# Kernel tuning notes

Measured on AMD Instinct MI355X. Metric: run time of the kernel, lower is better.

## Reference

```python
import jax, jax.numpy as jnp
import numpy as np

K = 5  # neighbors per node


def build_knn_adjacency(x, k=K):
    # x: (B, N, D) -> adj: (B, N, N)
    B, N, D = x.shape
    x_norm = x / jnp.clip(jnp.linalg.norm(x, axis=-1, keepdims=True), 1e-12)
    sim = jnp.einsum('bnd,bmd->bnm', x_norm, x_norm)  # (B, N, N)
    eye = jnp.eye(N, dtype=bool)
    sim = jnp.where(eye[None], jnp.asarray(-1.0, sim.dtype), sim)
    _, knn_idx = jax.lax.top_k(sim, k)  # (B, N, k)
    b_ix = jnp.arange(B)[:, None, None]
    i_ix = jnp.arange(N)[None, :, None]
    adj = jnp.zeros((B, N, N), dtype=x.dtype).at[b_ix, i_ix, knn_idx].set(1.0)
    adj = adj + jnp.eye(N, dtype=x.dtype)[None]
    return adj


def gcn_layer(x, adj, W, b):
    # deg-normalized aggregation then linear (torch Linear: x @ W.T + b)
    deg = adj.sum(axis=-1, keepdims=True)
    adj_norm = adj / jnp.clip(deg, 1.0)
    out = jnp.einsum('bnm,bmd->bnd', adj_norm, x)
    return out @ W.T + b


def setup_inputs() -> dict:
    key = jax.random.key(0)
    k1, k2, k3, k4, k5 = jax.random.split(key, 5)
    B, N, D, H = 32, 1024, 128, 128
    scale = 1.0 / np.sqrt(D)
    return {
        'x': jax.random.normal(k1, (B, N, D), dtype=jnp.float32),
        'W1': jax.random.normal(k2, (H, D), dtype=jnp.float32) * scale,
        'b1': jax.random.normal(k3, (H,), dtype=jnp.float32) * 0.01,
        'W2': jax.random.normal(k4, (H, H), dtype=jnp.float32) * scale,
        'b2': jax.random.normal(k5, (H,), dtype=jnp.float32) * 0.01,
    }


def reference(x, W1, b1, W2, b2):
    adj = build_knn_adjacency(x, k=K)
    h = x + jax.nn.relu(gcn_layer(x, adj, W1, b1))
    h = h + jax.nn.relu(gcn_layer(h, adj, W2, b2))
    return h  # pool='none' -> (B, N, hidden_dim)
```

## Files before the change

### kernel.cpp

```cpp
#include <hip/hip_runtime.h>
#include <float.h>
#include <math.h>

#define BB 32
#define NN 1024
#define DD 128
#define KK 5

typedef __attribute__((ext_vector_type(8))) short bf16x8;
typedef __attribute__((ext_vector_type(4))) float f32x4;

__device__ __forceinline__ unsigned short f2bf(float f) {
    unsigned int u = __float_as_uint(f);
    return (unsigned short)((u + 0x7FFFu + ((u >> 16) & 1u)) >> 16);
}
__device__ __forceinline__ float bf2f(unsigned short h) {
    return __uint_as_float(((unsigned int)h) << 16);
}

__global__ __launch_bounds__(256) void k_norm(const float* __restrict__ x,
                                              unsigned short* __restrict__ ph,
                                              unsigned short* __restrict__ pm,
                                              unsigned short* __restrict__ pl) {
    int row  = blockIdx.x * 4 + (threadIdx.x >> 6);
    int lane = threadIdx.x & 63;
    float2 v = *reinterpret_cast<const float2*>(x + (size_t)row * DD + lane * 2);
    float ss = v.x * v.x + v.y * v.y;
#pragma unroll
    for (int o = 32; o >= 1; o >>= 1) ss += __shfl_xor(ss, o);
    float inv = 1.0f / fmaxf(sqrtf(ss), 1e-12f);
    float y0 = v.x * inv, y1 = v.y * inv;

    unsigned short h0 = f2bf(y0);             float r0 = y0 - bf2f(h0);
    unsigned short m0 = f2bf(r0);             float s0 = r0 - bf2f(m0);
    unsigned short l0 = f2bf(s0);
    unsigned short h1 = f2bf(y1);             float r1 = y1 - bf2f(h1);
    unsigned short m1 = f2bf(r1);             float s1 = r1 - bf2f(m1);
    unsigned short l1 = f2bf(s1);

    size_t o = (size_t)row * DD + lane * 2;
    *reinterpret_cast<unsigned int*>(ph + o) = (unsigned int)h0 | ((unsigned int)h1 << 16);
    *reinterpret_cast<unsigned int*>(pm + o) = (unsigned int)m0 | ((unsigned int)m1 << 16);
    *reinterpret_cast<unsigned int*>(pl + o) = (unsigned int)l0 | ((unsigned int)l1 << 16);
}

union SMem {
    struct {
        unsigned short Ah[128][40], Am[128][40], Al[128][40];
        unsigned short Bh[128][40], Bm[128][40], Bl[128][40];
    } s;
    float q[4][32][68];
};

__device__ __forceinline__ void stage_plane(const unsigned short* __restrict__ g,
                                            unsigned short (*s)[40], int tid,
                                            size_t rowbase, int c) {
#pragma unroll
    for (int hh = 0; hh < 2; ++hh) {
        int u = tid + (hh << 8);
        int row = u >> 2, qq = u & 3;
        const float4 v = *reinterpret_cast<const float4*>(
            g + (rowbase + row) * DD + (c << 5) + (qq << 3));
        *reinterpret_cast<float4*>(&s[row][qq << 3]) = v;
    }
}

__global__ __launch_bounds__(256, 2) void k_sim(const unsigned short* __restrict__ ph,
                                                const unsigned short* __restrict__ pm,
                                                const unsigned short* __restrict__ pl,
                                                float* __restrict__ sim) {
    int bid = blockIdx.x;
    int lb  = (bid & 7) * 144 + (bid >> 3);
    int bl  = lb / 36;
    int p   = lb - bl * 36;
    int ti = 0;
    while (p >= 8 - ti) { p -= 8 - ti; ++ti; }
    int tj = ti + p;
    int R  = ti << 7, Cc = tj << 7;

    __shared__ SMem sm;

    int tid  = threadIdx.x;
    int wv   = tid >> 6;
    int lane = tid & 63;
    int wr = (wv >> 1) << 6;
    int wc = (wv & 1) << 6;
    int lg = lane >> 4, fr = lane & 15;

    size_t base = (size_t)bl * NN;
    size_t rbA = base + R, rbB = base + Cc;

    f32x4 acc[4][4];
#pragma unroll
    for (int i = 0; i < 4; ++i)
#pragma unroll
        for (int j = 0; j < 4; ++j) acc[i][j] = (f32x4){0.f, 0.f, 0.f, 0.f};

    int kk = lg << 3;

    for (int c = 0; c < 4; ++c) {
        if (c) __syncthreads();
        stage_plane(ph, sm.s.Ah, tid, rbA, c);
        stage_plane(pm, sm.s.Am, tid, rbA, c);
        stage_plane(pl, sm.s.Al, tid, rbA, c);
        stage_plane(ph, sm.s.Bh, tid, rbB, c);
        stage_plane(pm, sm.s.Bm, tid, rbB, c);
        stage_plane(pl, sm.s.Bl, tid, rbB, c);
        __syncthreads();

        bf16x8 bh[4], bm[4], blo[4];
#pragma unroll
        for (int cp = 0; cp < 4; ++cp) {
            int rb = wc + cp * 16 + fr;
            bh[cp]  = *reinterpret_cast<const bf16x8*>(&sm.s.Bh[rb][kk]);
            bm[cp]  = *reinterpret_cast<const bf16x8*>(&sm.s.Bm[rb][kk]);
            blo[cp] = *reinterpret_cast<const bf16x8*>(&sm.s.Bl[rb][kk]);
        }
#pragma unroll
        for (int rp = 0; rp < 4; ++rp) {
            int ra = wr + rp * 16 + fr;
            bf16x8 ah = *reinterpret_cast<const bf16x8*>(&sm.s.Ah[ra][kk]);
            bf16x8 am = *reinterpret_cast<const bf16x8*>(&sm.s.Am[ra][kk]);
            bf16x8 al = *reinterpret_cast<const bf16x8*>(&sm.s.Al[ra][kk]);
#pragma unroll
            for (int cp = 0; cp < 4; ++cp) {
                f32x4 cacc = acc[rp][cp];
                cacc = __builtin_amdgcn_mfma_f32_16x16x32_bf16(ah, bh[cp],  cacc, 0, 0, 0);
                cacc = __builtin_amdgcn_mfma_f32_16x16x32_bf16(ah, bm[cp],  cacc, 0, 0, 0);
                cacc = __builtin_amdgcn_mfma_f32_16x16x32_bf16(am, bh[cp],  cacc, 0, 0, 0);
                cacc = __builtin_amdgcn_mfma_f32_16x16x32_bf16(ah, blo[cp], cacc, 0, 0, 0);
                cacc = __builtin_amdgcn_mfma_f32_16x16x32_bf16(al, bh[cp],  cacc, 0, 0, 0);
                cacc = __builtin_amdgcn_mfma_f32_16x16x32_bf16(am, bm[cp],  cacc, 0, 0, 0);
                acc[rp][cp] = cacc;
            }
        }
    }

    __syncthreads();
    float (*q)[68] = sm.q[wv];
    float* Cb = sim + base * NN;

    if (ti != tj) {
#pragma unroll
        for (int hp = 0; hp < 2; ++hp) {
#pragma unroll
            for (int rp = 0; rp < 4; ++rp)
#pragma unroll
                for (int cpl = 0; cpl < 2; ++cpl) {
                    const f32x4 a = acc[rp][2 * hp + cpl];
                    *reinterpret_cast<float4*>(&q[cpl * 16 + fr][rp * 16 + lg * 4]) =
                        make_float4(a[0], a[1], a[2], a[3]);
                }
#pragma unroll
            for (int it = 0; it < 8; ++it) {
                int lcol = lg + 4 * it;
                const float4 v = *reinterpret_cast<const float4*>(&q[lcol][fr * 4]);
                *reinterpret_cast<float4*>(
                    &Cb[(size_t)(Cc + wc + 32 * hp + lcol) * NN + R + wr + fr * 4]) = v;
            }
        }
    }
#pragma unroll
    for (int hr = 0; hr < 2; ++hr) {
#pragma unroll
        for (int rpl = 0; rpl < 2; ++rpl)
#pragma unroll
            for (int cp = 0; cp < 4; ++cp)
#pragma unroll
                for (int reg = 0; reg < 4; ++reg)
                    q[rpl * 16 + lg * 4 + reg][cp * 16 + fr] = acc[2 * hr + rpl][cp][reg];
#pragma unroll
        for (int it = 0; it < 8; ++it) {
            int lrow = lg + 4 * it;
            const float4 v = *reinterpret_cast<const float4*>(&q[lrow][fr * 4]);
            *reinterpret_cast<float4*>(
                &Cb[(size_t)(R + wr + 32 * hr + lrow) * NN + Cc + wc + fr * 4]) = v;
        }
    }
}

__global__ __launch_bounds__(256) void k_topk(const float* __restrict__ sim,
                                              int* __restrict__ idx) {
    int lrow = blockIdx.x * 4 + (threadIdx.x >> 6);
    int lane = threadIdx.x & 63;
    const float* sr = sim + (size_t)lrow * NN;
    int i = lrow & (NN - 1);

    float v[16];
#pragma unroll
    for (int q = 0; q < 4; ++q) {
        float4 f = *reinterpret_cast<const float4*>(sr + lane * 16 + q * 4);
        v[q * 4 + 0] = f.x; v[q * 4 + 1] = f.y; v[q * 4 + 2] = f.z; v[q * 4 + 3] = f.w;
    }
    if ((i >> 4) == lane) {
        int s = i & 15;
#pragma unroll
        for (int j = 0; j < 16; ++j) if (j == s) v[j] = -FLT_MAX;
    }
    int* op = idx + (size_t)lrow * KK;
#pragma unroll
    for (int t = 0; t < KK; ++t) {
        float bv = v[0]; int bj = 0;
#pragma unroll
        for (int j = 1; j < 16; ++j) if (v[j] > bv) { bv = v[j]; bj = j; }
        int bm = (lane << 4) + bj;
#pragma unroll
        for (int o = 1; o < 64; o <<= 1) {
            float ov = __shfl_xor(bv, o);
            int   om = __shfl_xor(bm, o);
            if (ov > bv || (ov == bv && om < bm)) { bv = ov; bm = om; }
        }
        if ((bm >> 4) == lane) {
            int s = bm & 15;
#pragma unroll
            for (int j = 0; j < 16; ++j) if (j == s) v[j] = -FLT_MAX;
        }
        if (lane == 0) op[t] = bm;
    }
}

#define SW(c) ((c) + 4 * ((c) >> 5))

__global__ __launch_bounds__(256, 3) void k_gcn(const float* __restrict__ h,
                                                const int* __restrict__ idx,
                                                const float* __restrict__ W,
                                                const float* __restrict__ bias,
                                                const float* __restrict__ res,
                                                float* __restrict__ out) {
    int rt = blockIdx.x << 6;
    __shared__ float As[64][132];
    __shared__ float Bs[32][140];
    int tid = threadIdx.x;

    {
        int row = tid >> 2, fq = tid & 3;
        int grow = rt + row;
        const int* ip = idx + (size_t)grow * KK;
        const float* hb = h + (((size_t)grow >> 10) << 10) * DD;
        const float* hs = h + (size_t)grow * DD;
        int n0 = ip[0], n1 = ip[1], n2 = ip[2], n3 = ip[3], n4 = ip[4];
        const float* p0 = hb + (size_t)n0 * DD;
        const float* p1 = hb + (size_t)n1 * DD;
        const float* p2 = hb + (size_t)n2 * DD;
        const float* p3 = hb + (size_t)n3 * DD;
        const float* p4 = hb + (size_t)n4 * DD;
        const float cc = 1.0f / 6.0f;
#pragma unroll
        for (int rep = 0; rep < 8; ++rep) {
            int c = rep * 16 + fq * 4;
            float4 v  = *reinterpret_cast<const float4*>(hs + c);
            float4 u0 = *reinterpret_cast<const float4*>(p0 + c);
            float4 u1 = *reinterpret_cast<const float4*>(p1 + c);
            float4 u2 = *reinterpret_cast<const float4*>(p2 + c);
            float4 u3 = *reinterpret_cast<const float4*>(p3 + c);
            float4 u4 = *reinterpret_cast<const float4*>(p4 + c);
            v.x = (v.x + u0.x + u1.x + u2.x + u3.x + u4.x) * cc;
            v.y = (v.y + u0.y + u1.y + u2.y + u3.y + u4.y) * cc;
            v.z = (v.z + u0.z + u1.z + u2.z + u3.z + u4.z) * cc;
            v.w = (v.w + u0.w + u1.w + u2.w + u3.w + u4.w) * cc;
            *reinterpret_cast<float4*>(&As[row][c]) = v;
        }
    }

    int tr  = (tid >> 4) << 2;
    int tc  = (tid & 15) << 3;
    int stc = SW(tc);

    float acc[4][8];
#pragma unroll
    for (int i = 0; i < 4; ++i)
#pragma unroll
        for (int j = 0; j < 8; ++j) acc[i][j] = 0.f;

    for (int kc = 0; kc < 4; ++kc) {
        __syncthreads();
        {
            int hcol = tid >> 1, kq = tid & 1;
            int swc = SW(hcol);
#pragma unroll
            for (int rep = 0; rep < 4; ++rep) {
                int f4i = rep * 2 + kq;
                const float4 v = *reinterpret_cast<const float4*>(
                    W + (size_t)hcol * DD + kc * 32 + f4i * 4);
                int k = f4i * 4;
                Bs[k + 0][swc] = v.x; Bs[k + 1][swc] = v.y;
                Bs[k + 2][swc] = v.z; Bs[k + 3][swc] = v.w;
            }
        }
        __syncthreads();
#pragma unroll 4
        for (int k = 0; k < 32; ++k) {
            int ck = kc * 32 + k;
            const float av[4] = {As[tr + 0][ck], As[tr + 1][ck],
                                 As[tr + 2][ck], As[tr + 3][ck]};
            const float4 b0 = *reinterpret_cast<const float4*>(&Bs[k][stc]);
            const float4 b1 = *reinterpret_cast<const float4*>(&Bs[k][stc + 4]);
            const float bw[8] = {b0.x, b0.y, b0.z, b0.w, b1.x, b1.y, b1.z, b1.w};
#pragma unroll
            for (int ii = 0; ii < 4; ++ii)
#pragma unroll
                for (int jj = 0; jj < 8; ++jj)
                    acc[ii][jj] = fmaf(av[ii], bw[jj], acc[ii][jj]);
        }
    }
    const float4 bz0 = *reinterpret_cast<const float4*>(bias + tc);
    const float4 bz1 = *reinterpret_cast<const float4*>(bias + tc + 4);
    const float bb[8] = {bz0.x, bz0.y, bz0.z, bz0.w, bz1.x, bz1.y, bz1.z, bz1.w};
#pragma unroll
    for (int i = 0; i < 4; ++i) {
        size_t ro = (size_t)(rt + tr + i) * DD + tc;
        const float4 r0 = *reinterpret_cast<const float4*>(res + ro);
        const float4 r1 = *reinterpret_cast<const float4*>(res + ro + 4);
        float4 o0, o1;
        o0.x = r0.x + fmaxf(acc[i][0] + bb[0], 0.f);
        o0.y = r0.y + fmaxf(acc[i][1] + bb[1], 0.f);
        o0.z = r0.z + fmaxf(acc[i][2] + bb[2], 0.f);
        o0.w = r0.w + fmaxf(acc[i][3] + bb[3], 0.f);
        o1.x = r1.x + fmaxf(acc[i][4] + bb[4], 0.f);
        o1.y = r1.y + fmaxf(acc[i][5] + bb[5], 0.f);
        o1.z = r1.z + fmaxf(acc[i][6] + bb[6], 0.f);
        o1.w = r1.w + fmaxf(acc[i][7] + bb[7], 0.f);
        *reinterpret_cast<float4*>(out + ro)     = o0;
        *reinterpret_cast<float4*>(out + ro + 4) = o1;
    }
}

extern "C" void kernel_launch(void* const* d_in, const int* in_sizes, int n_in,
                              void* d_out, int out_size, void* d_ws, size_t ws_size,
                              hipStream_t stream) {
    const float* x  = (const float*)d_in[0];
    const float* W1 = (const float*)d_in[1];
    const float* b1 = (const float*)d_in[2];
    const float* W2 = (const float*)d_in[3];
    const float* b2 = (const float*)d_in[4];
    float* out = (float*)d_out;

    char* ws = (char*)d_ws;
    size_t pl_b  = (size_t)BB * NN * DD * 2;
    size_t h1_b  = (size_t)BB * NN * DD * 4;
    size_t idx_b = (size_t)BB * NN * KK * 4;
    unsigned short* ph = (unsigned short*)ws;  ws += pl_b;
    unsigned short* pm = (unsigned short*)ws;  ws += pl_b;
    unsigned short* pl = (unsigned short*)ws;  ws += pl_b;
    float* h1  = (float*)ws;                   ws += h1_b;
    int*   idx = (int*)ws;                     ws += idx_b;
    float* sim = (float*)ws;

    k_norm<<<BB * NN / 4, 256, 0, stream>>>(x, ph, pm, pl);
    k_sim<<<BB * 36, 256, 0, stream>>>(ph, pm, pl, sim);
    k_topk<<<BB * NN / 4, 256, 0, stream>>>(sim, idx);
    k_gcn<<<BB * NN / 64, 256, 0, stream>>>(x,  idx, W1, b1, x,  h1);
    k_gcn<<<BB * NN / 64, 256, 0, stream>>>(h1, idx, W2, b2, h1, out);
}
```

Measured before the change: 156.6 us.

## Fuse partial top-k into similarity kernel and merge candidates instead of storing sim

The similarity GEMM kernel no longer writes the full B×N×N similarity matrix. Each wave computes a per-row top-5 over its 64-column slice, for both the tile and its transpose, and writes packed 64-bit keys (value, column) as candidates. A new small merge kernel then reduces the 16 candidate lists per row to the final top-5 indices. This removes the 128MB sim write and reread, at the cost of extra shuffle and selection work in the GEMM epilogue.

```diff
diff --git a/kernel.cpp b/kernel.cpp
--- a/kernel.cpp
+++ b/kernel.cpp
@@ -9,6 +9,7 @@
 
 typedef __attribute__((ext_vector_type(8))) short bf16x8;
 typedef __attribute__((ext_vector_type(4))) float f32x4;
+typedef unsigned long long ull;
 
 __device__ __forceinline__ unsigned short f2bf(float f) {
     unsigned int u = __float_as_uint(f);
@@ -16,6 +17,12 @@
 }
 __device__ __forceinline__ float bf2f(unsigned short h) {
     return __uint_as_float(((unsigned int)h) << 16);
+}
+
+__device__ __forceinline__ ull mkkey(float v, int col) {
+    unsigned int u = __float_as_uint(v);
+    unsigned int ou = u ^ (unsigned)((((int)u) >> 31) | 0x80000000);
+    return ((ull)ou << 32) | (unsigned)(1023 - col);
 }
 
 __global__ __launch_bounds__(256) void k_norm(const float* __restrict__ x,
@@ -44,14 +51,6 @@
     *reinterpret_cast<unsigned int*>(pl + o) = (unsigned int)l0 | ((unsigned int)l1 << 16);
 }
 
-union SMem {
-    struct {
-        unsigned short Ah[128][40], Am[128][40], Al[128][40];
-        unsigned short Bh[128][40], Bm[128][40], Bl[128][40];
-    } s;
-    float q[4][32][68];
-};
-
 __device__ __forceinline__ void stage_plane(const unsigned short* __restrict__ g,
                                             unsigned short (*s)[40], int tid,
                                             size_t rowbase, int c) {
@@ -68,7 +67,7 @@
 __global__ __launch_bounds__(256, 2) void k_sim(const unsigned short* __restrict__ ph,
                                                 const unsigned short* __restrict__ pm,
                                                 const unsigned short* __restrict__ pl,
-                                                float* __restrict__ sim) {
+                                                ull* __restrict__ cand) {
     int bid = blockIdx.x;
     int lb  = (bid & 7) * 144 + (bid >> 3);
     int bl  = lb / 36;
@@ -78,7 +77,10 @@
     int tj = ti + p;
     int R  = ti << 7, Cc = tj << 7;
 
-    __shared__ SMem sm;
+    __shared__ struct {
+        unsigned short Ah[128][40], Am[128][40], Al[128][40];
+        unsigned short Bh[128][40], Bm[128][40], Bl[128][40];
+    } sm;
 
     int tid  = threadIdx.x;
     int wv   = tid >> 6;
@@ -100,28 +102,28 @@
 
     for (int c = 0; c < 4; ++c) {
         if (c) __syncthreads();
-        stage_plane(ph, sm.s.Ah, tid, rbA, c);
-        stage_plane(pm, sm.s.Am, tid, rbA, c);
-        stage_plane(pl, sm.s.Al, tid, rbA, c);
-        stage_plane(ph, sm.s.Bh, tid, rbB, c);
-        stage_plane(pm, sm.s.Bm, tid, rbB, c);
-        stage_plane(pl, sm.s.Bl, tid, rbB, c);
+        stage_plane(ph, sm.Ah, tid, rbA, c);
+        stage_plane(pm, sm.Am, tid, rbA, c);
+        stage_plane(pl, sm.Al, tid, rbA, c);
+        stage_plane(ph, sm.Bh, tid, rbB, c);
+        stage_plane(pm, sm.Bm, tid, rbB, c);
+        stage_plane(pl, sm.Bl, tid, rbB, c);
         __syncthreads();
 
         bf16x8 bh[4], bm[4], blo[4];
 #pragma unroll
         for (int cp = 0; cp < 4; ++cp) {
             int rb = wc + cp * 16 + fr;
-            bh[cp]  = *reinterpret_cast<const bf16x8*>(&sm.s.Bh[rb][kk]);
-            bm[cp]  = *reinterpret_cast<const bf16x8*>(&sm.s.Bm[rb][kk]);
-            blo[cp] = *reinterpret_cast<const bf16x8*>(&sm.s.Bl[rb][kk]);
+            bh[cp]  = *reinterpret_cast<const bf16x8*>(&sm.Bh[rb][kk]);
+            bm[cp]  = *reinterpret_cast<const bf16x8*>(&sm.Bm[rb][kk]);
+            blo[cp] = *reinterpret_cast<const bf16x8*>(&sm.Bl[rb][kk]);
         }
 #pragma unroll
         for (int rp = 0; rp < 4; ++rp) {
             int ra = wr + rp * 16 + fr;
-            bf16x8 ah = *reinterpret_cast<const bf16x8*>(&sm.s.Ah[ra][kk]);
-            bf16x8 am = *reinterpret_cast<const bf16x8*>(&sm.s.Am[ra][kk]);
-            bf16x8 al = *reinterpret_cast<const bf16x8*>(&sm.s.Al[ra][kk]);
+            bf16x8 ah = *reinterpret_cast<const bf16x8*>(&sm.Ah[ra][kk]);
+            bf16x8 am = *reinterpret_cast<const bf16x8*>(&sm.Am[ra][kk]);
+            bf16x8 al = *reinterpret_cast<const bf16x8*>(&sm.Al[ra][kk]);
 #pragma unroll
             for (int cp = 0; cp < 4; ++cp) {
                 f32x4 cacc = acc[rp][cp];
@@ -136,86 +138,107 @@
         }
     }
 
-    __syncthreads();
-    float (*q)[68] = sm.q[wv];
-    float* Cb = sim + base * NN;
+    {
+        int slotR = 2 * tj + (wc >> 6);
+        int c0 = Cc + wc + fr;
+#pragma unroll
+        for (int rp = 0; rp < 4; ++rp) {
+#pragma unroll
+            for (int reg = 0; reg < 4; ++reg) {
+                int grow = R + wr + rp * 16 + lg * 4 + reg;
+                float v0 = acc[rp][0][reg], v1 = acc[rp][1][reg];
+                float v2 = acc[rp][2][reg], v3 = acc[rp][3][reg];
+                if (ti == tj) {
+                    v0 = (c0      == grow) ? -FLT_MAX : v0;
+                    v1 = (c0 + 16 == grow) ? -FLT_MAX : v1;
+                    v2 = (c0 + 32 == grow) ? -FLT_MAX : v2;
+                    v3 = (c0 + 48 == grow) ? -FLT_MAX : v3;
+                }
+                ull w[5];
+#pragma unroll
+                for (int t = 0; t < 5; ++t) {
+                    float bv = v0; int bc = c0;
+                    if (v1 > bv) { bv = v1; bc = c0 + 16; }
+                    if (v2 > bv) { bv = v2; bc = c0 + 32; }
+                    if (v3 > bv) { bv = v3; bc = c0 + 48; }
+#pragma unroll
+                    for (int o = 1; o < 16; o <<= 1) {
+                        float ov = __shfl_xor(bv, o);
+                        int   oc = __shfl_xor(bc, o);
+                        if (ov > bv || (ov == bv && oc < bc)) { bv = ov; bc = oc; }
+                    }
+                    w[t] = mkkey(bv, bc);
+                    v0 = (bc == c0)      ? -FLT_MAX : v0;
+                    v1 = (bc == c0 + 16) ? -FLT_MAX : v1;
+                    v2 = (bc == c0 + 32) ? -FLT_MAX : v2;
+                    v3 = (bc == c0 + 48) ? -FLT_MAX : v3;
+                }
+                if (fr == 0) {
+                    ull* o = cand + ((base + grow) * 16 + slotR) * 5;
+                    o[0] = w[0]; o[1] = w[1]; o[2] = w[2]; o[3] = w[3]; o[4] = w[4];
+                }
+            }
+        }
+    }
 
     if (ti != tj) {
-#pragma unroll
-        for (int hp = 0; hp < 2; ++hp) {
+        int slotM = 2 * ti + (wr >> 6);
+        int nbase = R + wr + lg * 4;
+#pragma unroll
+        for (int cp = 0; cp < 4; ++cp) {
+            float mv[16];
 #pragma unroll
             for (int rp = 0; rp < 4; ++rp)
 #pragma unroll
-                for (int cpl = 0; cpl < 2; ++cpl) {
-                    const f32x4 a = acc[rp][2 * hp + cpl];
-                    *reinterpret_cast<float4*>(&q[cpl * 16 + fr][rp * 16 + lg * 4]) =
-                        make_float4(a[0], a[1], a[2], a[3]);
-                }
-#pragma unroll
-            for (int it = 0; it < 8; ++it) {
-                int lcol = lg + 4 * it;
-                const float4 v = *reinterpret_cast<const float4*>(&q[lcol][fr * 4]);
-                *reinterpret_cast<float4*>(
-                    &Cb[(size_t)(Cc + wc + 32 * hp + lcol) * NN + R + wr + fr * 4]) = v;
-            }
-        }
-    }
-#pragma unroll
-    for (int hr = 0; hr < 2; ++hr) {
-#pragma unroll
-        for (int rpl = 0; rpl < 2; ++rpl)
-#pragma unroll
-            for (int cp = 0; cp < 4; ++cp)
-#pragma unroll
                 for (int reg = 0; reg < 4; ++reg)
-                    q[rpl * 16 + lg * 4 + reg][cp * 16 + fr] = acc[2 * hr + rpl][cp][reg];
-#pragma unroll
-        for (int it = 0; it < 8; ++it) {
-            int lrow = lg + 4 * it;
-            const float4 v = *reinterpret_cast<const float4*>(&q[lrow][fr * 4]);
-            *reinterpret_cast<float4*>(
-                &Cb[(size_t)(R + wr + 32 * hr + lrow) * NN + Cc + wc + fr * 4]) = v;
-        }
-    }
-}
-
-__global__ __launch_bounds__(256) void k_topk(const float* __restrict__ sim,
-                                              int* __restrict__ idx) {
-    int lrow = blockIdx.x * 4 + (threadIdx.x >> 6);
-    int lane = threadIdx.x & 63;
-    const float* sr = sim + (size_t)lrow * NN;
-    int i = lrow & (NN - 1);
-
-    float v[16];
-#pragma unroll
-    for (int q = 0; q < 4; ++q) {
-        float4 f = *reinterpret_cast<const float4*>(sr + lane * 16 + q * 4);
-        v[q * 4 + 0] = f.x; v[q * 4 + 1] = f.y; v[q * 4 + 2] = f.z; v[q * 4 + 3] = f.w;
-    }
-    if ((i >> 4) == lane) {
-        int s = i & 15;
-#pragma unroll
-        for (int j = 0; j < 16; ++j) if (j == s) v[j] = -FLT_MAX;
-    }
-    int* op = idx + (size_t)lrow * KK;
-#pragma unroll
-    for (int t = 0; t < KK; ++t) {
-        float bv = v[0]; int bj = 0;
-#pragma unroll
-        for (int j = 1; j < 16; ++j) if (v[j] > bv) { bv = v[j]; bj = j; }
-        int bm = (lane << 4) + bj;
-#pragma unroll
-        for (int o = 1; o < 64; o <<= 1) {
-            float ov = __shfl_xor(bv, o);
-            int   om = __shfl_xor(bm, o);
-            if (ov > bv || (ov == bv && om < bm)) { bv = ov; bm = om; }
-        }
-        if ((bm >> 4) == lane) {
-            int s = bm & 15;
-#pragma unroll
-            for (int j = 0; j < 16; ++j) if (j == s) v[j] = -FLT_MAX;
-        }
-        if (lane == 0) op[t] = bm;
+                    mv[rp * 4 + reg] = acc[rp][cp][reg];
+            ull w[5];
+#pragma unroll
+            for (int t = 0; t < 5; ++t) {
+                float bv = mv[0]; int bn = nbase;
+#pragma unroll
+                for (int e = 1; e < 16; ++e) {
+                    int n = nbase + (e >> 2) * 16 + (e & 3);
+                    if (mv[e] > bv) { bv = mv[e]; bn = n; }
+                }
+                {   float ov = __shfl_xor(bv, 16); int on = __shfl_xor(bn, 16);
+                    if (ov > bv || (ov == bv && on < bn)) { bv = ov; bn = on; } }
+                {   float ov = __shfl_xor(bv, 32); int on = __shfl_xor(bn, 32);
+                    if (ov > bv || (ov == bv && on < bn)) { bv = ov; bn = on; } }
+                w[t] = mkkey(bv, bn);
+#pragma unroll
+                for (int e = 0; e < 16; ++e) {
+                    int n = nbase + (e >> 2) * 16 + (e & 3);
+                    mv[e] = (n == bn) ? -FLT_MAX : mv[e];
+                }
+            }
+            if (lg == 0) {
+                int node = Cc + wc + cp * 16 + fr;
+                ull* o = cand + ((base + node) * 16 + slotM) * 5;
+                o[0] = w[0]; o[1] = w[1]; o[2] = w[2]; o[3] = w[3]; o[4] = w[4];
+            }
+        }
+    }
+}
+
+__global__ __launch_bounds__(256) void k_merge(const ull* __restrict__ cand,
+                                               int* __restrict__ idx) {
+    int row = blockIdx.x * 16 + (threadIdx.x >> 4);
+    int g   = threadIdx.x & 15;
+    const ull* cp = cand + ((size_t)row * 16 + g) * 5;
+    ull k0 = cp[0], k1 = cp[1], k2 = cp[2], k3 = cp[3], k4 = cp[4];
+    int* op = idx + (size_t)row * KK;
+#pragma unroll
+    for (int t = 0; t < 5; ++t) {
+        ull w = k0;
+#pragma unroll
+        for (int o = 1; o < 16; o <<= 1) {
+            ull x = __shfl_xor(w, o); if (x > w) w = x;
+        }
+        if (g == t) op[t] = 1023 - (int)(w & 0xFFFFFFFFu);
+        bool adv = (k0 == w);
+        k0 = adv ? k1 : k0; k1 = adv ? k2 : k1;
+        k2 = adv ? k3 : k2; k3 = adv ? k4 : k3; k4 = adv ? 0ULL : k4;
     }
 }
 
@@ -336,19 +359,19 @@
     float* out = (float*)d_out;
 
     char* ws = (char*)d_ws;
-    size_t pl_b  = (size_t)BB * NN * DD * 2;
-    size_t h1_b  = (size_t)BB * NN * DD * 4;
-    size_t idx_b = (size_t)BB * NN * KK * 4;
+    size_t pl_b   = (size_t)BB * NN * DD * 2;
+    size_t h1_b   = (size_t)BB * NN * DD * 4;
+    size_t idx_b  = (size_t)BB * NN * KK * 4;
     unsigned short* ph = (unsigned short*)ws;  ws += pl_b;
     unsigned short* pm = (unsigned short*)ws;  ws += pl_b;
     unsigned short* pl = (unsigned short*)ws;  ws += pl_b;
     float* h1  = (float*)ws;                   ws += h1_b;
     int*   idx = (int*)ws;                     ws += idx_b;
-    float* sim = (float*)ws;
+    ull*  cand = (ull*)ws;
 
     k_norm<<<BB * NN / 4, 256, 0, stream>>>(x, ph, pm, pl);
-    k_sim<<<BB * 36, 256, 0, stream>>>(ph, pm, pl, sim);
-    k_topk<<<BB * NN / 4, 256, 0, stream>>>(sim, idx);
+    k_sim<<<BB * 36, 256, 0, stream>>>(ph, pm, pl, cand);
+    k_merge<<<BB * NN / 16, 256, 0, stream>>>(cand, idx);
     k_gcn<<<BB * NN / 64, 256, 0, stream>>>(x,  idx, W1, b1, x,  h1);
     k_gcn<<<BB * NN / 64, 256, 0, stream>>>(h1, idx, W2, b2, h1, out);
 }
```

New measurement: 221.0 us. 1.41x slower.

## Use split-bf16 MFMA for GCN linear layer instead of FP32 FMA

Applied to the files above, without the earlier changes.

Replaces the scalar FP32 register-tiled GEMM in k_gcn with bf16 MFMA 16x16x32 instructions. Each operand is split into hi and lo bf16 parts, and three MFMAs per tile (hh, hl, lh) approximate FP32 accuracy. W is read directly from global memory per wave instead of being staged through a shared-memory tile. The output is then staged through shared memory to give coalesced stores for the bias, ReLU and residual epilogue. The tradeoff is lower precision than pure FP32 and repeated global reads of W by each block.

```diff
diff --git a/kernel.cpp b/kernel.cpp
--- a/kernel.cpp
+++ b/kernel.cpp
@@ -16,6 +16,19 @@
 }
 __device__ __forceinline__ float bf2f(unsigned short h) {
     return __uint_as_float(((unsigned int)h) << 16);
+}
+
+__device__ __forceinline__ void split2(const float4& a0, const float4& a1,
+                                       bf16x8& hi, bf16x8& lo) {
+    float v[8] = {a0.x, a0.y, a0.z, a0.w, a1.x, a1.y, a1.z, a1.w};
+#pragma unroll
+    for (int j = 0; j < 8; ++j) {
+        unsigned short hb = f2bf(v[j]);
+        float r = v[j] - bf2f(hb);
+        unsigned short mb = f2bf(r);
+        hi[j] = (short)hb;
+        lo[j] = (short)mb;
+    }
 }
 
 __global__ __launch_bounds__(256) void k_norm(const float* __restrict__ x,
@@ -219,8 +232,6 @@
     }
 }
 
-#define SW(c) ((c) + 4 * ((c) >> 5))
-
 __global__ __launch_bounds__(256, 3) void k_gcn(const float* __restrict__ h,
                                                 const int* __restrict__ idx,
                                                 const float* __restrict__ W,
@@ -229,7 +240,6 @@
                                                 float* __restrict__ out) {
     int rt = blockIdx.x << 6;
     __shared__ float As[64][132];
-    __shared__ float Bs[32][140];
     int tid = threadIdx.x;
 
     {
@@ -261,67 +271,74 @@
             *reinterpret_cast<float4*>(&As[row][c]) = v;
         }
     }
-
-    int tr  = (tid >> 4) << 2;
-    int tc  = (tid & 15) << 3;
-    int stc = SW(tc);
-
-    float acc[4][8];
-#pragma unroll
-    for (int i = 0; i < 4; ++i)
-#pragma unroll
-        for (int j = 0; j < 8; ++j) acc[i][j] = 0.f;
-
+    __syncthreads();
+
+    int wv   = tid >> 6;
+    int lane = tid & 63;
+    int wr = (wv >> 1) << 5;
+    int wc = (wv & 1) << 6;
+    int lg = lane >> 4, fr = lane & 15;
+
+    f32x4 acc[2][4];
+#pragma unroll
+    for (int i = 0; i < 2; ++i)
+#pragma unroll
+        for (int j = 0; j < 4; ++j) acc[i][j] = (f32x4){0.f, 0.f, 0.f, 0.f};
+
+#pragma unroll
     for (int kc = 0; kc < 4; ++kc) {
-        __syncthreads();
-        {
-            int hcol = tid >> 1, kq = tid & 1;
-            int swc = SW(hcol);
-#pragma unroll
-            for (int rep = 0; rep < 4; ++rep) {
-                int f4i = rep * 2 + kq;
-                const float4 v = *reinterpret_cast<const float4*>(
-                    W + (size_t)hcol * DD + kc * 32 + f4i * 4);
-                int k = f4i * 4;
-                Bs[k + 0][swc] = v.x; Bs[k + 1][swc] = v.y;
-                Bs[k + 2][swc] = v.z; Bs[k + 3][swc] = v.w;
+        int k0 = kc * 32 + lg * 8;
+        bf16x8 ahh[2], ahm[2];
+#pragma unroll
+        for (int rp = 0; rp < 2; ++rp) {
+            const float* ap = &As[wr + rp * 16 + fr][k0];
+            split2(*reinterpret_cast<const float4*>(ap),
+                   *reinterpret_cast<const float4*>(ap + 4), ahh[rp], ahm[rp]);
+        }
+        bf16x8 bhh[4], bhm[4];
+#pragma unroll
+        for (int cp = 0; cp < 4; ++cp) {
+            const float* wp = W + (size_t)(wc + cp * 16 + fr) * DD + k0;
+            split2(*reinterpret_cast<const float4*>(wp),
+                   *reinterpret_cast<const float4*>(wp + 4), bhh[cp], bhm[cp]);
+        }
+#pragma unroll
+        for (int rp = 0; rp < 2; ++rp)
+#pragma unroll
+            for (int cp = 0; cp < 4; ++cp) {
+                f32x4 c = acc[rp][cp];
+                c = __builtin_amdgcn_mfma_f32_16x16x32_bf16(ahh[rp], bhh[cp], c, 0, 0, 0);
+                c = __builtin_amdgcn_mfma_f32_16x16x32_bf16(ahh[rp], bhm[cp], c, 0, 0, 0);
+                c = __builtin_amdgcn_mfma_f32_16x16x32_bf16(ahm[rp], bhh[cp], c, 0, 0, 0);
+                acc[rp][cp] = c;
             }
-        }
-        __syncthreads();
-#pragma unroll 4
-        for (int k = 0; k < 32; ++k) {
-            int ck = kc * 32 + k;
-            const float av[4] = {As[tr + 0][ck], As[tr + 1][ck],
-                                 As[tr + 2][ck], As[tr + 3][ck]};
-            const float4 b0 = *reinterpret_cast<const float4*>(&Bs[k][stc]);
-            const float4 b1 = *reinterpret_cast<const float4*>(&Bs[k][stc + 4]);
-            const float bw[8] = {b0.x, b0.y, b0.z, b0.w, b1.x, b1.y, b1.z, b1.w};
-#pragma unroll
-            for (int ii = 0; ii < 4; ++ii)
-#pragma unroll
-                for (int jj = 0; jj < 8; ++jj)
-                    acc[ii][jj] = fmaf(av[ii], bw[jj], acc[ii][jj]);
-        }
-    }
-    const float4 bz0 = *reinterpret_cast<const float4*>(bias + tc);
-    const float4 bz1 = *reinterpret_cast<const float4*>(bias + tc + 4);
-    const float bb[8] = {bz0.x, bz0.y, bz0.z, bz0.w, bz1.x, bz1.y, bz1.z, bz1.w};
-#pragma unroll
-    for (int i = 0; i < 4; ++i) {
-        size_t ro = (size_t)(rt + tr + i) * DD + tc;
-        const float4 r0 = *reinterpret_cast<const float4*>(res + ro);
-        const float4 r1 = *reinterpret_cast<const float4*>(res + ro + 4);
-        float4 o0, o1;
-        o0.x = r0.x + fmaxf(acc[i][0] + bb[0], 0.f);
-        o0.y = r0.y + fmaxf(acc[i][1] + bb[1], 0.f);
-        o0.z = r0.z + fmaxf(acc[i][2] + bb[2], 0.f);
-        o0.w = r0.w + fmaxf(acc[i][3] + bb[3], 0.f);
-        o1.x = r1.x + fmaxf(acc[i][4] + bb[4], 0.f);
-        o1.y = r1.y + fmaxf(acc[i][5] + bb[5], 0.f);
-        o1.z = r1.z + fmaxf(acc[i][6] + bb[6], 0.f);
-        o1.w = r1.w + fmaxf(acc[i][7] + bb[7], 0.f);
-        *reinterpret_cast<float4*>(out + ro)     = o0;
-        *reinterpret_cast<float4*>(out + ro + 4) = o1;
+    }
+
+    __syncthreads();
+#pragma unroll
+    for (int rp = 0; rp < 2; ++rp)
+#pragma unroll
+        for (int cp = 0; cp < 4; ++cp)
+#pragma unroll
+            for (int reg = 0; reg < 4; ++reg)
+                As[wr + rp * 16 + lg * 4 + reg][wc + cp * 16 + fr] = acc[rp][cp][reg];
+    __syncthreads();
+
+#pragma unroll
+    for (int rep = 0; rep < 8; ++rep) {
+        int slot = tid + rep * 256;
+        int row  = slot >> 5;
+        int c4   = (slot & 31) << 2;
+        float4 v  = *reinterpret_cast<const float4*>(&As[row][c4]);
+        size_t go = (size_t)(rt + row) * DD + c4;
+        const float4 r  = *reinterpret_cast<const float4*>(res + go);
+        const float4 bz = *reinterpret_cast<const float4*>(bias + c4);
+        float4 o;
+        o.x = r.x + fmaxf(v.x + bz.x, 0.f);
+        o.y = r.y + fmaxf(v.y + bz.y, 0.f);
+        o.z = r.z + fmaxf(v.z + bz.z, 0.f);
+        o.w = r.w + fmaxf(v.w + bz.w, 0.f);
+        *reinterpret_cast<float4*>(out + go) = o;
     }
 }
 
```

New measurement: 142.5 us (median of 2 runs). 9.0% less time.
